# Performance work log

Hardware: AMD Instinct MI355X
Metric: run time of the kernel (lower is better)

Reference implementation:

```python
import jax, jax.numpy as jnp
import numpy as np
import math

B, S, E, H = 4, 2048, 1024, 16
D = E // H
NEG_INF = -1e30  # stands in for -inf in masked_fill; softmax result identical for rows with valid entries


def setup_inputs() -> dict:
    key = jax.random.key(0)
    ks = jax.random.split(key, 7)
    sc = 1.0 / math.sqrt(E)
    return {
        "k": jax.random.normal(ks[0], (B, S, E), jnp.float32),
        "v": jax.random.normal(ks[1], (B, S, E), jnp.float32),
        "q": jax.random.normal(ks[2], (B, S, E), jnp.float32),
        "Wk": jax.random.normal(ks[3], (E, E), jnp.float32) * sc,
        "Wv": jax.random.normal(ks[4], (E, E), jnp.float32) * sc,
        "Wq": jax.random.normal(ks[5], (E, E), jnp.float32) * sc,
        "Wo": jax.random.normal(ks[6], (E, E), jnp.float32) * sc,
    }


def reference(k, v, q, Wk, Wv, Wq, Wo):
    # Linear(bias=False): y = x @ W.T
    kp = (k @ Wk.T).reshape(B, S, H, D).transpose(0, 2, 1, 3)  # [B,H,S,D]
    vp = (v @ Wv.T).reshape(B, S, H, D).transpose(0, 2, 1, 3)
    qp = (q @ Wq.T).reshape(B, S, H, D).transpose(0, 2, 1, 3)
    qp = qp / jnp.sqrt(jnp.asarray(D, qp.dtype))
    scores = jnp.einsum("bhqd,bhkd->bhqk", qp, kp)  # [B,H,S,S]
    causal = jnp.tril(jnp.ones((S, S), bool))  # [S,S]
    scores = jnp.where(causal[None, None], scores, NEG_INF)
    attn = jax.nn.softmax(scores, axis=-1)  # dropout p=0.0 (eval) -> identity
    out = jnp.einsum("bhqk,bhkd->bhqd", attn, vp)
    out = out.transpose(0, 2, 1, 3).reshape(B, S, E)
    return out @ Wo.T
```

## Files before the change

kernel.cpp:

```cpp
#include <hip/hip_runtime.h>

typedef __bf16 bf16_t;
typedef __bf16 bf16x8 __attribute__((ext_vector_type(8)));
typedef float f32x4 __attribute__((ext_vector_type(4)));
typedef float f32x16 __attribute__((ext_vector_type(16)));


__device__ __forceinline__ void async_copy16(const void* g, void* l) {
  __builtin_amdgcn_global_load_lds(
      (const __attribute__((address_space(1))) void*)g,
      (__attribute__((address_space(3))) void*)l, 16, 0, 0);
}

__device__ __forceinline__ unsigned pk_bf16(float lo, float hi) {
  unsigned r;
  asm("v_cvt_pk_bf16_f32 %0, %1, %2" : "=v"(r) : "v"(lo), "v"(hi));
  return r;
}

__global__ void cvt_all_kernel(const float* __restrict__ q, const float* __restrict__ k,
                               const float* __restrict__ v, const float* __restrict__ wk,
                               const float* __restrict__ wv, const float* __restrict__ wq,
                               const float* __restrict__ wo, uint2* __restrict__ out) {
  constexpr int QX = 2097152, QW = 262144;
  int g = blockIdx.x * 256 + threadIdx.x;
  const float* in; int off;
  if (g < QX)               { in = q;  off = 0; }
  else if (g < 2 * QX)      { in = k;  off = QX; }
  else if (g < 3 * QX)      { in = v;  off = 2 * QX; }
  else if (g < 3 * QX + QW)     { in = wk; off = 3 * QX; }
  else if (g < 3 * QX + 2 * QW) { in = wv; off = 3 * QX + QW; }
  else if (g < 3 * QX + 3 * QW) { in = wq; off = 3 * QX + 2 * QW; }
  else                          { in = wo; off = 3 * QX + 3 * QW; }
  float4 val = ((const float4*)in)[g - off];
  union { bf16_t h[4]; uint2 u; } cv;
  cv.h[0] = (bf16_t)val.x; cv.h[1] = (bf16_t)val.y;
  cv.h[2] = (bf16_t)val.z; cv.h[3] = (bf16_t)val.w;
  out[g] = cv.u;
}

__global__ __launch_bounds__(256) void qkv_kernel(
    const bf16_t* __restrict__ qb, const bf16_t* __restrict__ kb, const bf16_t* __restrict__ vb,
    const bf16_t* __restrict__ wqb, const bf16_t* __restrict__ wkb, const bf16_t* __restrict__ wvb,
    bf16_t* __restrict__ Qp, bf16_t* __restrict__ Kp, bf16_t* __restrict__ Vt, float qscale)
{
  constexpr int K = 1024;
  __shared__ __align__(16) bf16_t As[128 * 32];
  __shared__ __align__(16) bf16_t Bs[128 * 32];
  const int tid  = threadIdx.x;
  const int lane = tid & 63;
  const int wid  = tid >> 6;
  const int quad = lane >> 4;
  const int l16  = lane & 15;
  const int bx = blockIdx.x, by = blockIdx.y;
  const int sel = by >> 3, sub = by & 7;
  const bf16_t *X, *W; bf16_t* Y; float scale = 1.0f;
  int m0, n0;
  if (sel == 0)      { X = qb;  W = wqb; Y = Qp; m0 = bx * 128; n0 = sub * 128; scale = qscale; }
  else if (sel == 1) { X = kb;  W = wkb; Y = Kp; m0 = bx * 128; n0 = sub * 128; }
  else               { X = wvb; W = vb;  Y = Vt; m0 = sub * 128; n0 = bx * 128; }
  const int wm = (wid >> 1) * 64;
  const int wn = (wid & 1) * 64;
  const int swz = quad ^ ((l16 >> 1) & 3);

  f32x4 acc[4][4] = {};

  for (int k0 = 0; k0 < K; k0 += 32) {
#pragma unroll
    for (int p = 0; p < 2; ++p) {
      int c = tid + p * 256;
      int row = c >> 2;
      int seg = ((c & 3) ^ ((c >> 3) & 3)) * 8;
      async_copy16(&X[(size_t)(m0 + row) * K + k0 + seg], (char*)As + (p * 256 + wid * 64) * 16);
      async_copy16(&W[(size_t)(n0 + row) * K + k0 + seg], (char*)Bs + (p * 256 + wid * 64) * 16);
    }
    __syncthreads();
    bf16x8 af[4], bfr[4];
#pragma unroll
    for (int i = 0; i < 4; ++i)
      af[i] = *(const bf16x8*)((const char*)As + ((wm + i * 16 + l16) * 4 + swz) * 16);
#pragma unroll
    for (int j = 0; j < 4; ++j)
      bfr[j] = *(const bf16x8*)((const char*)Bs + ((wn + j * 16 + l16) * 4 + swz) * 16);
#pragma unroll
    for (int i = 0; i < 4; ++i)
#pragma unroll
      for (int j = 0; j < 4; ++j)
        acc[i][j] = __builtin_amdgcn_mfma_f32_16x16x32_bf16(af[i], bfr[j], acc[i][j], 0, 0, 0);
    __syncthreads();
  }

#pragma unroll
  for (int i = 0; i < 4; ++i)
#pragma unroll
    for (int j = 0; j < 4; ++j)
#pragma unroll
      for (int r = 0; r < 4; ++r) {
        int row = m0 + wm + i * 16 + quad * 4 + r;
        int col = n0 + wn + j * 16 + l16;
        float val = acc[i][j][r] * scale;
        if (sel < 2) {
          int b = row >> 11, s = row & 2047;
          int h = col >> 6,  d = col & 63;
          Y[(((size_t)(b * 16 + h) << 11) + s) * 64 + d] = (bf16_t)val;
        } else {
          int h = row >> 6,  d = row & 63;
          int b = col >> 11, s = col & 2047;
          Y[(((size_t)((b * 16 + h) * 64 + d)) << 11) + s] = (bf16_t)val;
        }
      }
}

__global__ __launch_bounds__(256) void out_gemm_kernel(
    const bf16_t* __restrict__ X, const bf16_t* __restrict__ W,
    float* __restrict__ Y, int M, int N, int K)
{
  __shared__ __align__(16) bf16_t As[128 * 32];
  __shared__ __align__(16) bf16_t Bs[128 * 32];
  const int tid  = threadIdx.x;
  const int lane = tid & 63;
  const int wid  = tid >> 6;
  const int quad = lane >> 4;
  const int l16  = lane & 15;
  const int m0 = blockIdx.x * 128;
  const int n0 = blockIdx.y * 128;
  const int wm = (wid >> 1) * 64;
  const int wn = (wid & 1) * 64;
  const int swz = quad ^ ((l16 >> 1) & 3);

  f32x4 acc[4][4] = {};

  for (int k0 = 0; k0 < K; k0 += 32) {
#pragma unroll
    for (int p = 0; p < 2; ++p) {
      int c = tid + p * 256;
      int row = c >> 2;
      int seg = ((c & 3) ^ ((c >> 3) & 3)) * 8;
      async_copy16(&X[(size_t)(m0 + row) * K + k0 + seg], (char*)As + (p * 256 + wid * 64) * 16);
      async_copy16(&W[(size_t)(n0 + row) * K + k0 + seg], (char*)Bs + (p * 256 + wid * 64) * 16);
    }
    __syncthreads();
    bf16x8 af[4], bfr[4];
#pragma unroll
    for (int i = 0; i < 4; ++i)
      af[i] = *(const bf16x8*)((const char*)As + ((wm + i * 16 + l16) * 4 + swz) * 16);
#pragma unroll
    for (int j = 0; j < 4; ++j)
      bfr[j] = *(const bf16x8*)((const char*)Bs + ((wn + j * 16 + l16) * 4 + swz) * 16);
#pragma unroll
    for (int i = 0; i < 4; ++i)
#pragma unroll
      for (int j = 0; j < 4; ++j)
        acc[i][j] = __builtin_amdgcn_mfma_f32_16x16x32_bf16(af[i], bfr[j], acc[i][j], 0, 0, 0);
    __syncthreads();
  }

#pragma unroll
  for (int i = 0; i < 4; ++i)
#pragma unroll
    for (int j = 0; j < 4; ++j)
#pragma unroll
      for (int r = 0; r < 4; ++r) {
        int row = m0 + wm + i * 16 + quad * 4 + r;
        int col = n0 + wn + j * 16 + l16;
        Y[(size_t)row * N + col] = acc[i][j][r];
      }
}

__global__ __launch_bounds__(256, 3) void attn_kernel(
    const bf16_t* __restrict__ Qp, const bf16_t* __restrict__ Kp,
    const bf16_t* __restrict__ Vt, bf16_t* __restrict__ O,
    float* __restrict__ Oacc, float* __restrict__ Racc)
{
  constexpr int S = 2048, D = 64, E = 1024;
  constexpr int BQ = 128, BK = 64;
  __shared__ __align__(16) bf16_t Ks[2][8 * 64 * 8];
  __shared__ __align__(16) bf16_t Vs[2][8 * 64 * 8];
  __shared__ float rsbuf[128];

  const int tid = threadIdx.x, lane = tid & 63, wid = tid >> 6;
  const int l31 = lane & 31, hi = lane >> 5;
  const int bh = blockIdx.y;
  const int b = bh >> 4, h = bh & 15;

  const int bx = blockIdx.x;
  int qt, s0, s1, half; bool direct;
  if (bx < 16) {
    qt = 15 - (bx >> 1);
    const int nks = 2 * qt + 2;
    half = bx & 1;
    s0 = half ? nks / 2 : 0;
    s1 = half ? nks : nks / 2;
    direct = false;
  } else {
    qt = 23 - bx;
    s0 = 0; s1 = 2 * qt + 2; half = 0;
    direct = true;
  }

  const int q0 = qt * BQ;
  const size_t base  = (size_t)bh * S * D;
  const size_t baseV = (size_t)bh * D * S;
  const int qmin = q0 + wid * 32;
  const int qmax = qmin + 31;

  bf16x8 qf[4];
#pragma unroll
  for (int ks = 0; ks < 4; ++ks)
    qf[ks] = *(const bf16x8*)&Qp[base + (size_t)(qmin + l31) * D + ks * 16 + hi * 8];

  {
    const int kb0 = s0 * BK;
#pragma unroll
    for (int is = 0; is < 2; ++is) {
      const int c = is * 256 + tid;
      const int p = c >> 6, row = c & 63;
      async_copy16(&Kp[base + (size_t)(kb0 + row) * D + p * 8],
                   (char*)Ks[s0 & 1] + (is * 256 + wid * 64) * 16);
      async_copy16(&Vt[baseV + (size_t)row * S + kb0 + p * 8],
                   (char*)Vs[s0 & 1] + (is * 256 + wid * 64) * 16);
    }
  }
  __syncthreads();

  const f32x16 z16 = {};
  f32x16 oa0 = {}, oa1 = {};
  float rs = 0.0f;

  for (int kt = s0; kt < s1; ++kt) {
    const int cur = kt & 1;
    const int k0 = kt * BK;
    if (kt + 1 < s1) {
      const int k0n = k0 + BK;
#pragma unroll
      for (int is = 0; is < 2; ++is) {
        const int c = is * 256 + tid;
        const int p = c >> 6, row = c & 63;
        async_copy16(&Kp[base + (size_t)(k0n + row) * D + p * 8],
                     (char*)Ks[cur ^ 1] + (is * 256 + wid * 64) * 16);
        async_copy16(&Vt[baseV + (size_t)row * S + k0n + p * 8],
                     (char*)Vs[cur ^ 1] + (is * 256 + wid * 64) * 16);
      }
    }
    if (k0 <= qmax) {
      const bf16_t* ksb = Ks[cur];
      const bf16_t* vsb = Vs[cur];
      f32x16 sc0, sc1;
      {
        const bf16x8 kf0 = *(const bf16x8*)&ksb[(hi * 64 + l31) * 8];
        const bf16x8 kf1 = *(const bf16x8*)&ksb[(hi * 64 + 32 + l31) * 8];
        sc0 = __builtin_amdgcn_mfma_f32_32x32x16_bf16(kf0, qf[0], z16, 0, 0, 0);
        sc1 = __builtin_amdgcn_mfma_f32_32x32x16_bf16(kf1, qf[0], z16, 0, 0, 0);
      }
#pragma unroll
      for (int ks = 1; ks < 4; ++ks) {
        const bf16x8 kf0 = *(const bf16x8*)&ksb[((ks * 2 + hi) * 64 + l31) * 8];
        const bf16x8 kf1 = *(const bf16x8*)&ksb[((ks * 2 + hi) * 64 + 32 + l31) * 8];
        sc0 = __builtin_amdgcn_mfma_f32_32x32x16_bf16(kf0, qf[ks], sc0, 0, 0, 0);
        sc1 = __builtin_amdgcn_mfma_f32_32x32x16_bf16(kf1, qf[ks], sc1, 0, 0, 0);
      }
      if (k0 + 63 > qmin) {
        const int qg = qmin + l31;
#pragma unroll
        for (int r = 0; r < 16; ++r) {
          const int kg = k0 + (r & 3) + 8 * (r >> 2) + 4 * hi;
          if (kg > qg)      sc0[r] = -1e30f;
          if (kg + 32 > qg) sc1[r] = -1e30f;
        }
      }
#pragma unroll
      for (int r = 0; r < 16; ++r) {
        sc0[r] = __builtin_amdgcn_exp2f(sc0[r]);
        sc1[r] = __builtin_amdgcn_exp2f(sc1[r]);
      }
      {
        float s0a = 0.f, s1a = 0.f, s2a = 0.f, s3a = 0.f;
#pragma unroll
        for (int r = 0; r < 16; r += 4) {
          s0a += sc0[r]     + sc1[r];
          s1a += sc0[r + 1] + sc1[r + 1];
          s2a += sc0[r + 2] + sc1[r + 2];
          s3a += sc0[r + 3] + sc1[r + 3];
        }
        rs += (s0a + s1a) + (s2a + s3a);
      }
      unsigned pw[16];
      {
        unsigned a0 = pk_bf16(sc0[0], sc0[1]),   a1 = pk_bf16(sc0[2], sc0[3]);
        unsigned b0 = pk_bf16(sc0[4], sc0[5]),   b1 = pk_bf16(sc0[6], sc0[7]);
        unsigned c0 = pk_bf16(sc0[8], sc0[9]),   c1 = pk_bf16(sc0[10], sc0[11]);
        unsigned d0 = pk_bf16(sc0[12], sc0[13]), d1 = pk_bf16(sc0[14], sc0[15]);
        asm("v_permlane32_swap_b32 %0, %1" : "+v"(a0), "+v"(b0));
        asm("v_permlane32_swap_b32 %0, %1" : "+v"(a1), "+v"(b1));
        asm("v_permlane32_swap_b32 %0, %1" : "+v"(c0), "+v"(d0));
        asm("v_permlane32_swap_b32 %0, %1" : "+v"(c1), "+v"(d1));
        pw[0] = a0; pw[1] = a1; pw[2] = b0; pw[3] = b1;
        pw[4] = c0; pw[5] = c1; pw[6] = d0; pw[7] = d1;
      }
      {
        unsigned a0 = pk_bf16(sc1[0], sc1[1]),   a1 = pk_bf16(sc1[2], sc1[3]);
        unsigned b0 = pk_bf16(sc1[4], sc1[5]),   b1 = pk_bf16(sc1[6], sc1[7]);
        unsigned c0 = pk_bf16(sc1[8], sc1[9]),   c1 = pk_bf16(sc1[10], sc1[11]);
        unsigned d0 = pk_bf16(sc1[12], sc1[13]), d1 = pk_bf16(sc1[14], sc1[15]);
        asm("v_permlane32_swap_b32 %0, %1" : "+v"(a0), "+v"(b0));
        asm("v_permlane32_swap_b32 %0, %1" : "+v"(a1), "+v"(b1));
        asm("v_permlane32_swap_b32 %0, %1" : "+v"(c0), "+v"(d0));
        asm("v_permlane32_swap_b32 %0, %1" : "+v"(c1), "+v"(d1));
        pw[8]  = a0; pw[9]  = a1; pw[10] = b0; pw[11] = b1;
        pw[12] = c0; pw[13] = c1; pw[14] = d0; pw[15] = d1;
      }
      union U8 { unsigned u[4]; bf16x8 v; };
#pragma unroll
      for (int kb = 0; kb < 2; ++kb)
#pragma unroll
        for (int ks2 = 0; ks2 < 2; ++ks2) {
          U8 pu;
          pu.u[0] = pw[kb * 8 + ks2 * 4 + 0];
          pu.u[1] = pw[kb * 8 + ks2 * 4 + 1];
          pu.u[2] = pw[kb * 8 + ks2 * 4 + 2];
          pu.u[3] = pw[kb * 8 + ks2 * 4 + 3];
          const int pnl = kb * 4 + ks2 * 2 + hi;
          const bf16x8 vf0 = *(const bf16x8*)&vsb[(pnl * 64 + l31) * 8];
          const bf16x8 vf1 = *(const bf16x8*)&vsb[(pnl * 64 + 32 + l31) * 8];
          oa0 = __builtin_amdgcn_mfma_f32_32x32x16_bf16(pu.v, vf0, oa0, 0, 0, 0);
          oa1 = __builtin_amdgcn_mfma_f32_32x32x16_bf16(pu.v, vf1, oa1, 0, 0, 0);
        }
    }
    __syncthreads();
  }

  const float full = rs + __shfl(rs, lane ^ 32);
  if (direct) {
    if (lane < 32) rsbuf[wid * 32 + l31] = full;
    __syncthreads();
#pragma unroll
    for (int r = 0; r < 16; ++r) {
      const int crow = (r & 3) + 8 * (r >> 2) + 4 * hi;
      const float inv = __builtin_amdgcn_rcpf(rsbuf[wid * 32 + crow]);
      const int row = q0 + wid * 32 + crow;
      const size_t rowoff = ((size_t)(b * S + row)) * E + h * D;
      O[rowoff + l31]      = (bf16_t)(oa0[r] * inv);
      O[rowoff + 32 + l31] = (bf16_t)(oa1[r] * inv);
    }
  } else {
    float* Oh = Oacc + (size_t)half * (64 * 1024 * 64);
    float* Rh = Racc + (size_t)half * (64 * 1024);
    if (lane < 32) Rh[(size_t)bh * 1024 + (qmin + l31 - 1024)] = full;
#pragma unroll
    for (int r = 0; r < 16; ++r) {
      const int crow = (r & 3) + 8 * (r >> 2) + 4 * hi;
      const int row = q0 + wid * 32 + crow;
      float* dst = &Oh[((size_t)bh * 1024 + (row - 1024)) * 64];
      dst[l31]      = oa0[r];
      dst[32 + l31] = oa1[r];
    }
  }
}

__global__ void attn_norm_kernel(const float* __restrict__ Oacc,
                                 const float* __restrict__ Racc,
                                 bf16_t* __restrict__ O) {
  constexpr size_t OHALF = (size_t)64 * 1024 * 64;
  constexpr size_t RHALF = (size_t)64 * 1024;
  const int g = blockIdx.x * 256 + threadIdx.x;
  const int r = g >> 4;
  const int dq = (g & 15) * 4;
  const int bh = r >> 10, srow = r & 1023;
  const int b = bh >> 4, h = bh & 15;
  const float4 v0 = *(const float4*)&Oacc[(size_t)r * 64 + dq];
  const float4 v1 = *(const float4*)&Oacc[OHALF + (size_t)r * 64 + dq];
  const float inv = __builtin_amdgcn_rcpf(Racc[r] + Racc[RHALF + r]);
  union { bf16_t hh[4]; uint2 u; } cv;
  cv.hh[0] = (bf16_t)((v0.x + v1.x) * inv);
  cv.hh[1] = (bf16_t)((v0.y + v1.y) * inv);
  cv.hh[2] = (bf16_t)((v0.z + v1.z) * inv);
  cv.hh[3] = (bf16_t)((v0.w + v1.w) * inv);
  const size_t off = ((size_t)(b * 2048 + 1024 + srow)) * 1024 + h * 64 + dq;
  *(uint2*)&O[off] = cv.u;
}

extern "C" void kernel_launch(void* const* d_in, const int* in_sizes, int n_in,
                              void* d_out, int out_size, void* d_ws, size_t ws_size,
                              hipStream_t stream) {
  const float* k_in = (const float*)d_in[0];
  const float* v_in = (const float*)d_in[1];
  const float* q_in = (const float*)d_in[2];
  const float* Wk_in = (const float*)d_in[3];
  const float* Wv_in = (const float*)d_in[4];
  const float* Wq_in = (const float*)d_in[5];
  const float* Wo_in = (const float*)d_in[6];
  float* out = (float*)d_out;

  constexpr int    M = 8192, N = 1024, K = 1024;
  constexpr size_t SZ_X = (size_t)M * K * 2;
  constexpr size_t SZ_W = (size_t)N * K * 2;

  char* ws = (char*)d_ws;
  bf16_t* qb  = (bf16_t*)(ws);
  bf16_t* kb  = (bf16_t*)(ws + SZ_X);
  bf16_t* vb  = (bf16_t*)(ws + 2 * SZ_X);
  bf16_t* wkb = (bf16_t*)(ws + 3 * SZ_X);
  bf16_t* wvb = (bf16_t*)(ws + 3 * SZ_X + SZ_W);
  bf16_t* wqb = (bf16_t*)(ws + 3 * SZ_X + 2 * SZ_W);
  bf16_t* wob = (bf16_t*)(ws + 3 * SZ_X + 3 * SZ_W);
  bf16_t* Qp  = (bf16_t*)(ws + 3 * SZ_X + 4 * SZ_W);
  bf16_t* Kp  = (bf16_t*)(ws + 4 * SZ_X + 4 * SZ_W);
  bf16_t* Vtg = (bf16_t*)(ws + 5 * SZ_X + 4 * SZ_W);
  bf16_t* Ob  = qb;
  float* Oacc = (float*)(ws + SZ_X);
  float* Racc = (float*)(ws + 3 * SZ_X);

  cvt_all_kernel<<<28672, 256, 0, stream>>>(q_in, k_in, v_in, Wk_in, Wv_in, Wq_in, Wo_in,
                                            (uint2*)ws);

  qkv_kernel<<<dim3(64, 24), 256, 0, stream>>>(qb, kb, vb, wqb, wkb, wvb,
                                               Qp, Kp, Vtg, 0.125f * 1.44269504f);

  attn_kernel<<<dim3(24, 4 * 16), 256, 0, stream>>>(Qp, Kp, Vtg, Ob, Oacc, Racc);

  attn_norm_kernel<<<4096, 256, 0, stream>>>(Oacc, Racc, Ob);

  out_gemm_kernel<<<dim3(M / 128, N / 128), 256, 0, stream>>>(Ob, wob, out, M, N, K);
}
```

Measured before the change: 325.4 us.

## Split K/V staging into a deeper pipeline and reorder attention block scheduling

```diff
diff --git a/kernel.cpp b/kernel.cpp
--- a/kernel.cpp
+++ b/kernel.cpp
@@ -174,29 +174,24 @@
 {
   constexpr int S = 2048, D = 64, E = 1024;
   constexpr int BQ = 128, BK = 64;
-  __shared__ __align__(16) bf16_t Ks[2][8 * 64 * 8];
+  __shared__ __align__(16) bf16_t Ks[3][8 * 64 * 8];
   __shared__ __align__(16) bf16_t Vs[2][8 * 64 * 8];
-  __shared__ float rsbuf[128];
+  float* rsbuf = (float*)Ks;
 
   const int tid = threadIdx.x, lane = tid & 63, wid = tid >> 6;
   const int l31 = lane & 31, hi = lane >> 5;
-  const int bh = blockIdx.y;
+
+  const signed char QT_TAB[24] = {15,15,7,14,14,13,13,6,12,12,11,11,5,10,10,9,9,4,8,8,3,2,1,0};
+  const signed char HF_TAB[24] = {0,1,2,0,1,0,1,2,0,1,0,1,2,0,1,0,1,2,0,1,2,2,2,2};
+  const int rank = (int)blockIdx.x >> 6;
+  const int bh   = (int)blockIdx.x & 63;
   const int b = bh >> 4, h = bh & 15;
-
-  const int bx = blockIdx.x;
-  int qt, s0, s1, half; bool direct;
-  if (bx < 16) {
-    qt = 15 - (bx >> 1);
-    const int nks = 2 * qt + 2;
-    half = bx & 1;
-    s0 = half ? nks / 2 : 0;
-    s1 = half ? nks : nks / 2;
-    direct = false;
-  } else {
-    qt = 23 - bx;
-    s0 = 0; s1 = 2 * qt + 2; half = 0;
-    direct = true;
-  }
+  const int qt = QT_TAB[rank];
+  const int hf = HF_TAB[rank];
+  const int nks = 2 * qt + 2;
+  int s0, s1, half; bool direct;
+  if (hf == 2) { s0 = 0; s1 = nks; half = 0; direct = true; }
+  else         { half = hf; s0 = half ? nks / 2 : 0; s1 = half ? nks : nks / 2; direct = false; }
 
   const int q0 = qt * BQ;
   const size_t base  = (size_t)bh * S * D;
@@ -209,42 +204,46 @@
   for (int ks = 0; ks < 4; ++ks)
     qf[ks] = *(const bf16x8*)&Qp[base + (size_t)(qmin + l31) * D + ks * 16 + hi * 8];
 
-  {
-    const int kb0 = s0 * BK;
+  auto stageK = [&](int kt, int buf) {
 #pragma unroll
     for (int is = 0; is < 2; ++is) {
       const int c = is * 256 + tid;
       const int p = c >> 6, row = c & 63;
-      async_copy16(&Kp[base + (size_t)(kb0 + row) * D + p * 8],
-                   (char*)Ks[s0 & 1] + (is * 256 + wid * 64) * 16);
-      async_copy16(&Vt[baseV + (size_t)row * S + kb0 + p * 8],
-                   (char*)Vs[s0 & 1] + (is * 256 + wid * 64) * 16);
-    }
-  }
-  __syncthreads();
+      async_copy16(&Kp[base + (size_t)(kt * BK + row) * D + p * 8],
+                   (char*)Ks[buf] + (is * 256 + wid * 64) * 16);
+    }
+  };
+  auto stageV = [&](int kt, int buf) {
+#pragma unroll
+    for (int is = 0; is < 2; ++is) {
+      const int c = is * 256 + tid;
+      const int p = c >> 6, row = c & 63;
+      async_copy16(&Vt[baseV + (size_t)row * S + kt * BK + p * 8],
+                   (char*)Vs[buf] + (is * 256 + wid * 64) * 16);
+    }
+  };
+
+  stageK(s0, s0 % 3);
+  stageV(s0, s0 & 1);
+  if (s0 + 1 < s1) stageK(s0 + 1, (s0 + 1) % 3);
 
   const f32x16 z16 = {};
   f32x16 oa0 = {}, oa1 = {};
   float rs = 0.0f;
 
   for (int kt = s0; kt < s1; ++kt) {
-    const int cur = kt & 1;
     const int k0 = kt * BK;
-    if (kt + 1 < s1) {
-      const int k0n = k0 + BK;
-#pragma unroll
-      for (int is = 0; is < 2; ++is) {
-        const int c = is * 256 + tid;
-        const int p = c >> 6, row = c & 63;
-        async_copy16(&Kp[base + (size_t)(k0n + row) * D + p * 8],
-                     (char*)Ks[cur ^ 1] + (is * 256 + wid * 64) * 16);
-        async_copy16(&Vt[baseV + (size_t)row * S + k0n + p * 8],
-                     (char*)Vs[cur ^ 1] + (is * 256 + wid * 64) * 16);
-      }
-    }
-    if (k0 <= qmax) {
-      const bf16_t* ksb = Ks[cur];
-      const bf16_t* vsb = Vs[cur];
+    const bool live = (k0 <= qmax);
+    if (kt + 1 < s1) { asm volatile("s_waitcnt vmcnt(4)" ::: "memory"); }
+    else             { asm volatile("s_waitcnt vmcnt(2)" ::: "memory"); }
+    __builtin_amdgcn_s_barrier();
+    __builtin_amdgcn_sched_barrier(0);
+    if (kt + 1 < s1) stageV(kt + 1, (kt + 1) & 1);
+    if (kt + 2 < s1) stageK(kt + 2, (kt + 2) % 3);
+
+    unsigned pw[16];
+    if (live) {
+      const bf16_t* ksb = Ks[kt % 3];
       f32x16 sc0, sc1;
       {
         const bf16x8 kf0 = *(const bf16x8*)&ksb[(hi * 64 + l31) * 8];
@@ -284,7 +283,6 @@
         }
         rs += (s0a + s1a) + (s2a + s3a);
       }
-      unsigned pw[16];
       {
         unsigned a0 = pk_bf16(sc0[0], sc0[1]),   a1 = pk_bf16(sc0[2], sc0[3]);
         unsigned b0 = pk_bf16(sc0[4], sc0[5]),   b1 = pk_bf16(sc0[6], sc0[7]);
@@ -309,6 +307,14 @@
         pw[8]  = a0; pw[9]  = a1; pw[10] = b0; pw[11] = b1;
         pw[12] = c0; pw[13] = c1; pw[14] = d0; pw[15] = d1;
       }
+    }
+    if (kt + 2 < s1)      { asm volatile("s_waitcnt vmcnt(6)" ::: "memory"); }
+    else if (kt + 1 < s1) { asm volatile("s_waitcnt vmcnt(4)" ::: "memory"); }
+    else                  { asm volatile("s_waitcnt vmcnt(0)" ::: "memory"); }
+    __builtin_amdgcn_s_barrier();
+    __builtin_amdgcn_sched_barrier(0);
+    if (live) {
+      const bf16_t* vsb = Vs[kt & 1];
       union U8 { unsigned u[4]; bf16x8 v; };
 #pragma unroll
       for (int kb = 0; kb < 2; ++kb)
@@ -326,11 +332,11 @@
           oa1 = __builtin_amdgcn_mfma_f32_32x32x16_bf16(pu.v, vf1, oa1, 0, 0, 0);
         }
     }
-    __syncthreads();
   }
 
   const float full = rs + __shfl(rs, lane ^ 32);
   if (direct) {
+    __syncthreads();
     if (lane < 32) rsbuf[wid * 32 + l31] = full;
     __syncthreads();
 #pragma unroll
@@ -416,7 +422,7 @@
   qkv_kernel<<<dim3(64, 24), 256, 0, stream>>>(qb, kb, vb, wqb, wkb, wvb,
                                                Qp, Kp, Vtg, 0.125f * 1.44269504f);
 
-  attn_kernel<<<dim3(24, 4 * 16), 256, 0, stream>>>(Qp, Kp, Vtg, Ob, Oacc, Racc);
+  attn_kernel<<<dim3(1536), 256, 0, stream>>>(Qp, Kp, Vtg, Ob, Oacc, Racc);
 
   attn_norm_kernel<<<4096, 256, 0, stream>>>(Oacc, Racc, Ob);
 
```

Result: faster. 307.2 us (median of 2 runs) (-5.6%).
